# Kernel tuning notes

Measured on AMD Instinct MI355X. Metric: run time of the kernel, lower is better.

## Reference

```python
import jax, jax.numpy as jnp
import numpy as np

N, D_IN = 65536, 512
H1, H2, D_SH = 1024, 1024, 512   # shared net: num_nodes_shared = [1024, 1024, 512]
HI = 512                          # indiv hidden width, num_nodes_indiv = [512, 512]


def setup_inputs() -> dict:
    key = jax.random.key(0)
    ks = jax.random.split(key, 16)
    s = 0.02
    inp = {
        "input": jax.random.normal(ks[0], (N, D_IN), jnp.float32),
        "treatment": jax.random.randint(ks[1], (N,), 0, 2, jnp.int32),
        # shared net (hidden ReLU layers + linear output, all with bias)
        "W0": jax.random.normal(ks[2], (D_IN, H1), jnp.float32) * s,
        "b0": jnp.zeros((H1,), jnp.float32),
        "W1": jax.random.normal(ks[3], (H1, H2), jnp.float32) * s,
        "b1": jnp.zeros((H2,), jnp.float32),
        "W2": jax.random.normal(ks[4], (H2, D_SH), jnp.float32) * s,
        "b2": jnp.zeros((D_SH,), jnp.float32),
        # risk net 0 (output layer has no bias)
        "A0": jax.random.normal(ks[5], (D_SH, HI), jnp.float32) * s,
        "a0": jnp.zeros((HI,), jnp.float32),
        "A1": jax.random.normal(ks[6], (HI, HI), jnp.float32) * s,
        "a1": jnp.zeros((HI,), jnp.float32),
        "A2": jax.random.normal(ks[7], (HI, 1), jnp.float32) * s,
        # risk net 1
        "C0": jax.random.normal(ks[8], (D_SH, HI), jnp.float32) * s,
        "c0": jnp.zeros((HI,), jnp.float32),
        "C1": jax.random.normal(ks[9], (HI, HI), jnp.float32) * s,
        "c1": jnp.zeros((HI,), jnp.float32),
        "C2": jax.random.normal(ks[10], (HI, 1), jnp.float32) * s,
    }
    return inp


def _risk_net(h, U0, u0, U1, u1, U2):
    h = jax.nn.relu(h @ U0 + u0)
    h = jax.nn.relu(h @ U1 + u1)
    return h @ U2  # [N, 1], no output bias


def reference(input, treatment, W0, b0, W1, b1, W2, b2,
              A0, a0, A1, a1, A2, C0, c0, C1, c1, C2):
    # shared MLP
    h = jax.nn.relu(input @ W0 + b0)
    h = jax.nn.relu(h @ W1 + b1)
    out = h @ W2 + b2                     # [N, D_SH]
    # Binary expert routing. The torch code gathers samples per treatment,
    # runs each group through its own MLP and scatters results back; the
    # math is equivalent to applying both experts and selecting per sample.
    y0 = _risk_net(out, A0, a0, A1, a1, A2)[:, 0]  # [N]
    y1 = _risk_net(out, C0, c0, C1, c1, C2)[:, 0]  # [N]
    y = jnp.where(treatment == 0, y0, y1)          # [N]
    return (y, out)
```

## Files before the change

### kernel.cpp

```cpp
#include <hip/hip_runtime.h>
#include <hip/hip_bf16.h>
#include <stdint.h>

typedef short short8 __attribute__((ext_vector_type(8)));
typedef float f32x4 __attribute__((ext_vector_type(4)));

#define NSAMP 65536
#define AS1 __attribute__((address_space(1)))
#define AS3 __attribute__((address_space(3)))

__device__ __forceinline__ unsigned f2bf(float f) {
    union { float f; unsigned u; } v; v.f = f;
    unsigned u = v.u;
    u += 0x7fffu + ((u >> 16) & 1u);
    return u >> 16;
}

__device__ __forceinline__ void wr8(char* d, f32x4 a, f32x4 b) {
    short8 o;
    o[0] = (short)f2bf(a[0]); o[1] = (short)f2bf(a[1]);
    o[2] = (short)f2bf(a[2]); o[3] = (short)f2bf(a[3]);
    o[4] = (short)f2bf(b[0]); o[5] = (short)f2bf(b[1]);
    o[6] = (short)f2bf(b[2]); o[7] = (short)f2bf(b[3]);
    *(short8*)d = o;
}

struct PrepArgs {
    const float *W0, *W1, *W2, *A0, *C0, *A1, *C1, *a0v, *c0v;
    unsigned short *W0T, *W1T, *W2T, *RT0, *A1T, *C1T;
    float *bcat, *yout;
};
__global__ void k_prep(PrepArgs p) {
    int i = blockIdx.x * blockDim.x + threadIdx.x;
    if (i < 524288)  { int k = i >> 10, n = i & 1023; p.W0T[n * 512 + k] = f2bf(p.W0[i]); return; }
    i -= 524288;
    if (i < 1048576) { int k = i >> 10, n = i & 1023; p.W1T[n * 1024 + k] = f2bf(p.W1[i]); return; }
    i -= 1048576;
    if (i < 524288)  { int k = i >> 9, n = i & 511; p.W2T[n * 1024 + k] = f2bf(p.W2[i]); return; }
    i -= 524288;
    if (i < 262144)  { int k = i >> 9, n = i & 511; p.RT0[n * 512 + k] = f2bf(p.A0[i]); return; }
    i -= 262144;
    if (i < 262144)  { int k = i >> 9, n = i & 511; p.RT0[(512 + n) * 512 + k] = f2bf(p.C0[i]); return; }
    i -= 262144;
    if (i < 262144)  { int k = i >> 9, n = i & 511; p.A1T[n * 512 + k] = f2bf(p.A1[i]); return; }
    i -= 262144;
    if (i < 262144)  { int k = i >> 9, n = i & 511; p.C1T[n * 512 + k] = f2bf(p.C1[i]); return; }
    i -= 262144;
    if (i < 512)     { p.bcat[i] = p.a0v[i]; return; }
    i -= 512;
    if (i < 512)     { p.bcat[512 + i] = p.c0v[i]; return; }
    i -= 512;
    if (i < 65536)   { p.yout[i] = 0.f; return; }
}

template<int MODE>
__global__ __launch_bounds__(512, 2)
void k_gemm256(const void* __restrict__ Av, int lda,
               const unsigned short* __restrict__ BT, const unsigned short* __restrict__ BT2,
               const float* __restrict__ bias, const float* __restrict__ bias2,
               unsigned short* __restrict__ Cbf, float* __restrict__ Cf32,
               const float* __restrict__ w2, const float* __restrict__ w2b,
               const int* __restrict__ TRt, float* __restrict__ ydot,
               int Ncols, int K, int TPB)
{
    __shared__ __align__(16) char lds[65536];

    const int tid  = threadIdx.x;
    const int lane = tid & 63;
    const int wid  = tid >> 6;
    const int wr   = wid >> 2;
    const int wcn  = wid & 3;

    const int bid  = (int)((blockIdx.x & 7) * 64 + (blockIdx.x >> 3));
    const int cls  = bid % TPB;
    const int w    = bid / TPB;
    const int NBPC = 512 / TPB;
    const int TAUS = 256 / NBPC;

    int n0e, cOff = 0, expert = 0;
    const unsigned short* Bsel = BT;
    if (MODE == 2) {
        expert = cls >> 1;
        n0e = (cls & 1) << 8;
        cOff = expert << 9;
        if (expert) Bsel = BT2;
    } else {
        n0e = cls << 8;
    }

    const int srow = tid >> 2;
    const int scs  = (tid & 3) ^ ((srow >> 1) & 3);
    const int ldst = wid * 1024;

    const unsigned short* gB0 = Bsel + (size_t)(n0e + srow) * K + scs * 8;
    const unsigned short* gB1 = gB0 + (size_t)128 * K;

    const unsigned short* Ab = (const unsigned short*)Av;
    const float*          Af = (const float*)Av;
    const size_t dA = (size_t)NBPC * 256 * lda;
    const unsigned short* cA0 = Ab + (size_t)((w << 8) + srow) * lda + cOff + scs * 8;
    const unsigned short* cA1 = cA0 + (size_t)128 * lda;

    const int arow = tid >> 1;
    const int hh   = (tid & 1) * 2;
    const int xw   = (arow >> 1) & 3;
    const float* cFa = Af + (size_t)((w << 8) + arow) * lda + (size_t)(hh ^ xw) * 8;
    const float* cFb = Af + (size_t)((w << 8) + arow) * lda + (size_t)((hh + 1) ^ xw) * 8;

#define STAGE_A(db, pA0, pA1, ko)                                                        \
    do {                                                                                 \
        __builtin_amdgcn_global_load_lds((const AS1 void*)((pA0) + (ko)),                \
                                         (AS3 void*)((db) + ldst), 16, 0, 0);            \
        __builtin_amdgcn_global_load_lds((const AS1 void*)((pA1) + (ko)),                \
                                         (AS3 void*)((db) + 8192 + ldst), 16, 0, 0);     \
    } while (0)
#define STAGE_B(db, ko)                                                                  \
    do {                                                                                 \
        __builtin_amdgcn_global_load_lds((const AS1 void*)(gB0 + (ko)),                  \
                                         (AS3 void*)((db) + 16384 + ldst), 16, 0, 0);    \
        __builtin_amdgcn_global_load_lds((const AS1 void*)(gB1 + (ko)),                  \
                                         (AS3 void*)((db) + 24576 + ldst), 16, 0, 0);    \
    } while (0)

    int aOff[8], bOff[4];
#pragma unroll
    for (int i = 0; i < 8; ++i) {
        int r = wr * 128 + i * 16 + (lane & 15);
        aOff[i] = r * 64 + ((((lane >> 4) ^ ((r >> 1) & 3))) << 4);
    }
#pragma unroll
    for (int j = 0; j < 4; ++j) {
        int r = wcn * 64 + j * 16 + (lane & 15);
        bOff[j] = r * 64 + ((((lane >> 4) ^ ((r >> 1) & 3))) << 4);
    }

    f32x4 acc[8][4];
#pragma unroll
    for (int i = 0; i < 8; ++i)
#pragma unroll
        for (int j = 0; j < 4; ++j) acc[i][j] = (f32x4)0.f;

    const int KT  = K >> 5;
    const int TOT = TAUS * KT;

    f32x4 xr0, xr1, xr2, xr3;

    if constexpr (MODE == 3) {
        f32x4 a0 = *(const f32x4*)(cFa);
        f32x4 a1 = *(const f32x4*)(cFa + 4);
        f32x4 a2 = *(const f32x4*)(cFb);
        f32x4 a3 = *(const f32x4*)(cFb + 4);
        STAGE_B(lds, 0);
        wr8(lds + tid * 32, a0, a1);
        wr8(lds + tid * 32 + 16, a2, a3);
        xr0 = *(const f32x4*)(cFa + 32); xr1 = *(const f32x4*)(cFa + 36);
        xr2 = *(const f32x4*)(cFb + 32); xr3 = *(const f32x4*)(cFb + 36);
    } else {
        STAGE_A(lds, cA0, cA1, 0);
        STAGE_B(lds, 0);
    }

    int g = 0;
    for (int tau = 0; tau < TAUS; ++tau) {
        const unsigned short* nA0 = cA0 + dA;
        const unsigned short* nA1 = cA1 + dA;
        const float* nFa = cFa + dA;
        const float* nFb = cFb + dA;

        for (int t = 0; t < KT; ++t, ++g) {
            const char* sbuf = lds + (g & 1) * 32768;
            char* dbuf = lds + ((g + 1) & 1) * 32768;
            const bool st  = (g + 1 < TOT);
            const bool st2 = (g + 2 < TOT);
            const bool inTile = (t + 1 < KT);
            const int kb1 = inTile ? ((t + 1) << 5) : 0;

            if constexpr (MODE == 3) {
                if (st) {
                    wr8(dbuf + tid * 32, xr0, xr1);
                    wr8(dbuf + tid * 32 + 16, xr2, xr3);
                    STAGE_B(dbuf, kb1);
                } else {
                    asm volatile("s_waitcnt vmcnt(0)" ::: "memory");
                }
                if (st2) {
                    const float* Fa2 = cFa; const float* Fb2 = cFb;
                    int t2 = t + 2, k2;
                    if (t2 >= KT) { t2 -= KT; Fa2 = nFa; Fb2 = nFb; }
                    k2 = t2 << 5;
                    xr0 = *(const f32x4*)(Fa2 + k2);     xr1 = *(const f32x4*)(Fa2 + k2 + 4);
                    xr2 = *(const f32x4*)(Fb2 + k2);     xr3 = *(const f32x4*)(Fb2 + k2 + 4);
                }
                asm volatile("s_waitcnt lgkmcnt(0)" ::: "memory");
                __builtin_amdgcn_sched_barrier(0);
            } else {
                if (st) {
                    const unsigned short* sA0 = inTile ? cA0 : nA0;
                    const unsigned short* sA1 = inTile ? cA1 : nA1;
                    STAGE_A(dbuf, sA0, sA1, kb1);
                    STAGE_B(dbuf, kb1);
                    asm volatile("s_waitcnt vmcnt(4)" ::: "memory");
                } else {
                    asm volatile("s_waitcnt vmcnt(0)" ::: "memory");
                }
                __builtin_amdgcn_sched_barrier(0);
            }
            __builtin_amdgcn_s_barrier();
            __builtin_amdgcn_sched_barrier(0);

            short8 fa[8], fb[4];
#pragma unroll
            for (int i = 0; i < 8; ++i) fa[i] = *(const short8*)(sbuf + aOff[i]);
#pragma unroll
            for (int j = 0; j < 4; ++j) fb[j] = *(const short8*)(sbuf + 16384 + bOff[j]);
            __builtin_amdgcn_s_setprio(1);
#pragma unroll
            for (int i = 0; i < 8; ++i)
#pragma unroll
                for (int j = 0; j < 4; ++j)
                    acc[i][j] = __builtin_amdgcn_mfma_f32_16x16x32_bf16(fb[j], fa[i], acc[i][j], 0, 0, 0);
            __builtin_amdgcn_s_setprio(0);
            __builtin_amdgcn_s_barrier();
        }

        const int m0 = (w + NBPC * tau) << 8;
        if (MODE == 2) {
            const float* be = expert ? bias2 : bias;
            const float* we = expert ? w2b : w2;
            const int nb = n0e + wcn * 64 + ((lane >> 4) << 2);
            f32x4 bv[4], wv[4];
#pragma unroll
            for (int j = 0; j < 4; ++j) {
                bv[j] = *(const f32x4*)(be + nb + j * 16);
                wv[j] = *(const f32x4*)(we + nb + j * 16);
            }
#pragma unroll
            for (int i = 0; i < 8; ++i) {
                float p = 0.f;
#pragma unroll
                for (int j = 0; j < 4; ++j)
#pragma unroll
                    for (int r = 0; r < 4; ++r)
                        p += fmaxf(acc[i][j][r] + bv[j][r], 0.f) * wv[j][r];
                p += __shfl_xor(p, 16);
                p += __shfl_xor(p, 32);
                const int m = m0 + wr * 128 + i * 16 + (lane & 15);
                if (lane < 16 && TRt[m] == expert) atomicAdd(&ydot[m], p);
            }
        } else {
            const int nb = n0e + wcn * 64 + ((lane >> 4) << 2);
            f32x4 bv[4];
#pragma unroll
            for (int j = 0; j < 4; ++j) bv[j] = *(const f32x4*)(bias + nb + j * 16);
#pragma unroll
            for (int i = 0; i < 8; ++i) {
                const int m = m0 + wr * 128 + i * 16 + (lane & 15);
                unsigned short* pbc = Cbf + (size_t)m * Ncols + nb;
#pragma unroll
                for (int j = 0; j < 4; ++j) {
                    f32x4 v = acc[i][j] + bv[j];
                    if (MODE != 1) {
#pragma unroll
                        for (int r = 0; r < 4; ++r) v[r] = fmaxf(v[r], 0.f);
                    }
                    if (MODE == 1) *(f32x4*)(Cf32 + (size_t)m * Ncols + nb + j * 16) = v;
                    unsigned long long pk =
                        (unsigned long long)(f2bf(v[0]) | (f2bf(v[1]) << 16)) |
                        ((unsigned long long)(f2bf(v[2]) | (f2bf(v[3]) << 16)) << 32);
                    *(unsigned long long*)(pbc + j * 16) = pk;
                }
            }
        }

#pragma unroll
        for (int i = 0; i < 8; ++i)
#pragma unroll
            for (int j = 0; j < 4; ++j) acc[i][j] = (f32x4)0.f;
        cA0 = nA0; cA1 = nA1; cFa = nFa; cFb = nFb;
    }
#undef STAGE_A
#undef STAGE_B
}


extern "C" void kernel_launch(void* const* d_in, const int* in_sizes, int n_in,
                              void* d_out, int out_size, void* d_ws, size_t ws_size,
                              hipStream_t stream) {
    const float* X  = (const float*)d_in[0];
    const int*  TR  = (const int*)d_in[1];
    const float* W0 = (const float*)d_in[2];  const float* b0 = (const float*)d_in[3];
    const float* W1 = (const float*)d_in[4];  const float* b1 = (const float*)d_in[5];
    const float* W2 = (const float*)d_in[6];  const float* b2 = (const float*)d_in[7];
    const float* A0 = (const float*)d_in[8];  const float* a0 = (const float*)d_in[9];
    const float* A1 = (const float*)d_in[10]; const float* a1 = (const float*)d_in[11];
    const float* A2 = (const float*)d_in[12];
    const float* C0 = (const float*)d_in[13]; const float* c0 = (const float*)d_in[14];
    const float* C1 = (const float*)d_in[15]; const float* c1 = (const float*)d_in[16];
    const float* C2 = (const float*)d_in[17];

    float* y_out   = (float*)d_out;
    float* out_out = (float*)d_out + NSAMP;

    char* ws = (char*)d_ws;
    size_t off = 0;
    auto alloc = [&](size_t bytes) -> char* {
        char* p = ws + off;
        off += (bytes + 255) & ~(size_t)255;
        return p;
    };
    unsigned short* H1b = (unsigned short*)alloc((size_t)NSAMP * 1024 * 2);
    unsigned short* H2b = (unsigned short*)alloc((size_t)NSAMP * 1024 * 2);
    unsigned short* OUTb = H1b;
    unsigned short* R01  = H2b;
    unsigned short* W0T = (unsigned short*)alloc(512 * 1024 * 2);
    unsigned short* W1T = (unsigned short*)alloc(1024 * 1024 * 2);
    unsigned short* W2T = (unsigned short*)alloc(1024 * 512 * 2);
    unsigned short* RT0 = (unsigned short*)alloc(1024 * 512 * 2);
    unsigned short* A1T = (unsigned short*)alloc(512 * 512 * 2);
    unsigned short* C1T = (unsigned short*)alloc(512 * 512 * 2);
    float* bcat = (float*)alloc(1024 * 4);

    PrepArgs pa;
    pa.W0 = W0; pa.W1 = W1; pa.W2 = W2; pa.A0 = A0; pa.C0 = C0; pa.A1 = A1; pa.C1 = C1;
    pa.a0v = a0; pa.c0v = c0;
    pa.W0T = W0T; pa.W1T = W1T; pa.W2T = W2T; pa.RT0 = RT0; pa.A1T = A1T; pa.C1T = C1T;
    pa.bcat = bcat; pa.yout = y_out;
    k_prep<<<(3212288 + 255) / 256, 256, 0, stream>>>(pa);

    k_gemm256<3><<<512, 512, 0, stream>>>((const void*)X, 512, W0T, nullptr, b0, nullptr,
                                          H1b, nullptr, nullptr, nullptr, nullptr, nullptr,
                                          1024, 512, 4);
    k_gemm256<0><<<512, 512, 0, stream>>>((const void*)H1b, 1024, W1T, nullptr, b1, nullptr,
                                          H2b, nullptr, nullptr, nullptr, nullptr, nullptr,
                                          1024, 1024, 4);
    k_gemm256<1><<<512, 512, 0, stream>>>((const void*)H2b, 1024, W2T, nullptr, b2, nullptr,
                                          OUTb, out_out, nullptr, nullptr, nullptr, nullptr,
                                          512, 1024, 2);

    k_gemm256<0><<<512, 512, 0, stream>>>((const void*)OUTb, 512, RT0, nullptr, bcat, nullptr,
                                          R01, nullptr, nullptr, nullptr, nullptr, nullptr,
                                          1024, 512, 4);

    k_gemm256<2><<<512, 512, 0, stream>>>((const void*)R01, 1024, A1T, C1T, a1, c1,
                                          nullptr, nullptr, A2, C2, TR, y_out,
                                          512, 512, 4);
}
```

Baseline: 599.2 us.

## Triple-buffer LDS with register fragment prefetch and one block per CU

Replaces the double-buffered LDS pipeline with three 32KB stages (96KB LDS), so global loads are issued two k-steps ahead. It prefetches the next tile's B and first-half A fragments into registers while the current MFMAs run, and drops one barrier per iteration. The grid shrinks from 512 to 256 persistent blocks with launch_bounds occupancy 1, so each block covers more M tiles. The trade is lower occupancy and more register pressure in exchange for deeper software pipelining and less synchronisation.

```diff
diff --git a/kernel.cpp b/kernel.cpp
--- a/kernel.cpp
+++ b/kernel.cpp
@@ -54,7 +54,7 @@
 }
 
 template<int MODE>
-__global__ __launch_bounds__(512, 2)
+__global__ __launch_bounds__(512)
 void k_gemm256(const void* __restrict__ Av, int lda,
                const unsigned short* __restrict__ BT, const unsigned short* __restrict__ BT2,
                const float* __restrict__ bias, const float* __restrict__ bias2,
@@ -63,7 +63,7 @@
                const int* __restrict__ TRt, float* __restrict__ ydot,
                int Ncols, int K, int TPB)
 {
-    __shared__ __align__(16) char lds[65536];
+    __shared__ __align__(16) char lds[98304];
 
     const int tid  = threadIdx.x;
     const int lane = tid & 63;
@@ -71,11 +71,10 @@
     const int wr   = wid >> 2;
     const int wcn  = wid & 3;
 
-    const int bid  = (int)((blockIdx.x & 7) * 64 + (blockIdx.x >> 3));
-    const int cls  = bid % TPB;
-    const int w    = bid / TPB;
-    const int NBPC = 512 / TPB;
-    const int TAUS = 256 / NBPC;
+    const int bid   = (int)((blockIdx.x & 7) * 32 + (blockIdx.x >> 3));
+    const int cls   = bid % TPB;
+    const int w     = bid / TPB;
+    const int MSTEP = 256 / TPB;
 
     int n0e, cOff = 0, expert = 0;
     const unsigned short* Bsel = BT;
@@ -97,7 +96,7 @@
 
     const unsigned short* Ab = (const unsigned short*)Av;
     const float*          Af = (const float*)Av;
-    const size_t dA = (size_t)NBPC * 256 * lda;
+    const size_t dA = (size_t)MSTEP * 256 * lda;
     const unsigned short* cA0 = Ab + (size_t)((w << 8) + srow) * lda + cOff + scs * 8;
     const unsigned short* cA1 = cA0 + (size_t)128 * lda;
 
@@ -141,89 +140,113 @@
         for (int j = 0; j < 4; ++j) acc[i][j] = (f32x4)0.f;
 
     const int KT  = K >> 5;
-    const int TOT = TAUS * KT;
+    const int TOT = TPB * KT;
+
+    char* pR = lds;
+    char* pN = lds + 32768;
+    char* pS = lds + 65536;
 
     f32x4 xr0, xr1, xr2, xr3;
 
     if constexpr (MODE == 3) {
-        f32x4 a0 = *(const f32x4*)(cFa);
-        f32x4 a1 = *(const f32x4*)(cFa + 4);
-        f32x4 a2 = *(const f32x4*)(cFb);
-        f32x4 a3 = *(const f32x4*)(cFb + 4);
-        STAGE_B(lds, 0);
-        wr8(lds + tid * 32, a0, a1);
-        wr8(lds + tid * 32 + 16, a2, a3);
+        f32x4 a0 = *(const f32x4*)(cFa);     f32x4 a1p = *(const f32x4*)(cFa + 4);
+        f32x4 a2 = *(const f32x4*)(cFb);     f32x4 a3p = *(const f32x4*)(cFb + 4);
+        STAGE_B(pR, 0);
         xr0 = *(const f32x4*)(cFa + 32); xr1 = *(const f32x4*)(cFa + 36);
         xr2 = *(const f32x4*)(cFb + 32); xr3 = *(const f32x4*)(cFb + 36);
+        STAGE_B(pN, 32);
+        wr8(pR + tid * 32, a0, a1p);
+        wr8(pR + tid * 32 + 16, a2, a3p);
+        asm volatile("s_waitcnt vmcnt(6)" ::: "memory");
     } else {
-        STAGE_A(lds, cA0, cA1, 0);
-        STAGE_B(lds, 0);
-    }
+        STAGE_A(pR, cA0, cA1, 0);
+        STAGE_B(pR, 0);
+        STAGE_A(pN, cA0, cA1, 32);
+        STAGE_B(pN, 32);
+        asm volatile("s_waitcnt vmcnt(4)" ::: "memory");
+    }
+    asm volatile("s_waitcnt lgkmcnt(0)" ::: "memory");
+    __builtin_amdgcn_s_barrier();
+    __builtin_amdgcn_sched_barrier(0);
+
+    short8 fb[4], fa0[4], fa1[4], nfb[4], nfa0[4];
+#pragma unroll
+    for (int j = 0; j < 4; ++j) fb[j]  = *(const short8*)(pR + 16384 + bOff[j]);
+#pragma unroll
+    for (int i = 0; i < 4; ++i) fa0[i] = *(const short8*)(pR + aOff[i]);
 
     int g = 0;
-    for (int tau = 0; tau < TAUS; ++tau) {
+    for (int tau = 0; tau < TPB; ++tau) {
         const unsigned short* nA0 = cA0 + dA;
         const unsigned short* nA1 = cA1 + dA;
         const float* nFa = cFa + dA;
         const float* nFb = cFb + dA;
 
         for (int t = 0; t < KT; ++t, ++g) {
-            const char* sbuf = lds + (g & 1) * 32768;
-            char* dbuf = lds + ((g + 1) & 1) * 32768;
-            const bool st  = (g + 1 < TOT);
-            const bool st2 = (g + 2 < TOT);
-            const bool inTile = (t + 1 < KT);
-            const int kb1 = inTile ? ((t + 1) << 5) : 0;
+            const bool stN = (g + 1 < TOT);
+            const bool stS = (g + 2 < TOT);
+            const int  t2  = t + 2;
+            const bool in2 = (t2 < KT);
+            const int  kb2 = (in2 ? t2 : t2 - KT) << 5;
 
             if constexpr (MODE == 3) {
-                if (st) {
-                    wr8(dbuf + tid * 32, xr0, xr1);
-                    wr8(dbuf + tid * 32 + 16, xr2, xr3);
-                    STAGE_B(dbuf, kb1);
+                if (stN) {
+                    wr8(pN + tid * 32, xr0, xr1);
+                    wr8(pN + tid * 32 + 16, xr2, xr3);
+                }
+            }
+#pragma unroll
+            for (int i = 0; i < 4; ++i) fa1[i] = *(const short8*)(pR + aOff[4 + i]);
+            if (stS) {
+                if constexpr (MODE == 3) {
+                    const float* Fa2 = in2 ? cFa : nFa;
+                    const float* Fb2 = in2 ? cFb : nFb;
+                    xr0 = *(const f32x4*)(Fa2 + kb2);     xr1 = *(const f32x4*)(Fa2 + kb2 + 4);
+                    xr2 = *(const f32x4*)(Fb2 + kb2);     xr3 = *(const f32x4*)(Fb2 + kb2 + 4);
+                    STAGE_B(pS, kb2);
+                    asm volatile("s_waitcnt vmcnt(6)" ::: "memory");
                 } else {
-                    asm volatile("s_waitcnt vmcnt(0)" ::: "memory");
+                    const unsigned short* sA0 = in2 ? cA0 : nA0;
+                    const unsigned short* sA1 = in2 ? cA1 : nA1;
+                    STAGE_A(pS, sA0, sA1, kb2);
+                    STAGE_B(pS, kb2);
+                    asm volatile("s_waitcnt vmcnt(4)" ::: "memory");
                 }
-                if (st2) {
-                    const float* Fa2 = cFa; const float* Fb2 = cFb;
-                    int t2 = t + 2, k2;
-                    if (t2 >= KT) { t2 -= KT; Fa2 = nFa; Fb2 = nFb; }
-                    k2 = t2 << 5;
-                    xr0 = *(const f32x4*)(Fa2 + k2);     xr1 = *(const f32x4*)(Fa2 + k2 + 4);
-                    xr2 = *(const f32x4*)(Fb2 + k2);     xr3 = *(const f32x4*)(Fb2 + k2 + 4);
-                }
-                asm volatile("s_waitcnt lgkmcnt(0)" ::: "memory");
-                __builtin_amdgcn_sched_barrier(0);
             } else {
-                if (st) {
-                    const unsigned short* sA0 = inTile ? cA0 : nA0;
-                    const unsigned short* sA1 = inTile ? cA1 : nA1;
-                    STAGE_A(dbuf, sA0, sA1, kb1);
-                    STAGE_B(dbuf, kb1);
-                    asm volatile("s_waitcnt vmcnt(4)" ::: "memory");
-                } else {
-                    asm volatile("s_waitcnt vmcnt(0)" ::: "memory");
-                }
-                __builtin_amdgcn_sched_barrier(0);
-            }
+                asm volatile("s_waitcnt vmcnt(0)" ::: "memory");
+            }
+            asm volatile("s_waitcnt lgkmcnt(0)" ::: "memory");
+            __builtin_amdgcn_sched_barrier(0);
             __builtin_amdgcn_s_barrier();
             __builtin_amdgcn_sched_barrier(0);
 
-            short8 fa[8], fb[4];
-#pragma unroll
-            for (int i = 0; i < 8; ++i) fa[i] = *(const short8*)(sbuf + aOff[i]);
-#pragma unroll
-            for (int j = 0; j < 4; ++j) fb[j] = *(const short8*)(sbuf + 16384 + bOff[j]);
+            if (stN) {
+#pragma unroll
+                for (int j = 0; j < 4; ++j) nfb[j]  = *(const short8*)(pN + 16384 + bOff[j]);
+#pragma unroll
+                for (int i = 0; i < 4; ++i) nfa0[i] = *(const short8*)(pN + aOff[i]);
+            }
             __builtin_amdgcn_s_setprio(1);
 #pragma unroll
-            for (int i = 0; i < 8; ++i)
+            for (int i = 0; i < 4; ++i)
 #pragma unroll
                 for (int j = 0; j < 4; ++j)
-                    acc[i][j] = __builtin_amdgcn_mfma_f32_16x16x32_bf16(fb[j], fa[i], acc[i][j], 0, 0, 0);
+                    acc[i][j] = __builtin_amdgcn_mfma_f32_16x16x32_bf16(fb[j], fa0[i], acc[i][j], 0, 0, 0);
+#pragma unroll
+            for (int i = 0; i < 4; ++i)
+#pragma unroll
+                for (int j = 0; j < 4; ++j)
+                    acc[4 + i][j] = __builtin_amdgcn_mfma_f32_16x16x32_bf16(fb[j], fa1[i], acc[4 + i][j], 0, 0, 0);
             __builtin_amdgcn_s_setprio(0);
-            __builtin_amdgcn_s_barrier();
+
+#pragma unroll
+            for (int j = 0; j < 4; ++j) fb[j] = nfb[j];
+#pragma unroll
+            for (int i = 0; i < 4; ++i) fa0[i] = nfa0[i];
+            char* tmp = pR; pR = pN; pN = pS; pS = tmp;
         }
 
-        const int m0 = (w + NBPC * tau) << 8;
+        const int m0 = (w + MSTEP * tau) << 8;
         if (MODE == 2) {
             const float* be = expert ? bias2 : bias;
             const float* we = expert ? w2b : w2;
@@ -327,21 +350,21 @@
     pa.bcat = bcat; pa.yout = y_out;
     k_prep<<<(3212288 + 255) / 256, 256, 0, stream>>>(pa);
 
-    k_gemm256<3><<<512, 512, 0, stream>>>((const void*)X, 512, W0T, nullptr, b0, nullptr,
+    k_gemm256<3><<<256, 512, 0, stream>>>((const void*)X, 512, W0T, nullptr, b0, nullptr,
                                           H1b, nullptr, nullptr, nullptr, nullptr, nullptr,
                                           1024, 512, 4);
-    k_gemm256<0><<<512, 512, 0, stream>>>((const void*)H1b, 1024, W1T, nullptr, b1, nullptr,
+    k_gemm256<0><<<256, 512, 0, stream>>>((const void*)H1b, 1024, W1T, nullptr, b1, nullptr,
                                           H2b, nullptr, nullptr, nullptr, nullptr, nullptr,
                                           1024, 1024, 4);
-    k_gemm256<1><<<512, 512, 0, stream>>>((const void*)H2b, 1024, W2T, nullptr, b2, nullptr,
+    k_gemm256<1><<<256, 512, 0, stream>>>((const void*)H2b, 1024, W2T, nullptr, b2, nullptr,
                                           OUTb, out_out, nullptr, nullptr, nullptr, nullptr,
                                           512, 1024, 2);
 
-    k_gemm256<0><<<512, 512, 0, stream>>>((const void*)OUTb, 512, RT0, nullptr, bcat, nullptr,
+    k_gemm256<0><<<256, 512, 0, stream>>>((const void*)OUTb, 512, RT0, nullptr, bcat, nullptr,
                                           R01, nullptr, nullptr, nullptr, nullptr, nullptr,
                                           1024, 512, 4);
 
-    k_gemm256<2><<<512, 512, 0, stream>>>((const void*)R01, 1024, A1T, C1T, a1, c1,
+    k_gemm256<2><<<256, 512, 0, stream>>>((const void*)R01, 1024, A1T, C1T, a1, c1,
                                           nullptr, nullptr, A2, C2, TR, y_out,
                                           512, 512, 4);
 }
```

Result: faster. 569.8 us (-4.9%).
